# Performance work log

Hardware: AMD Instinct MI355X
Metric: run time of the kernel (lower is better)

## Reference

```python
import jax, jax.numpy as jnp
import numpy as np

IN_F = 128
OUT_F = 128
N_NODES = 50000
N_EDGES = 800000


def setup_inputs() -> dict:
    key = jax.random.key(0)
    k_x, k_e, k_w, k_b = jax.random.split(key, 4)
    x = jax.random.normal(k_x, (N_NODES, IN_F), dtype=jnp.float32)
    edge_index = jax.random.randint(k_e, (2, N_EDGES), 0, N_NODES, dtype=jnp.int64)
    # linear params (torch nn.Linear: y = x @ W.T + b)
    bound = 1.0 / np.sqrt(IN_F)
    W = jax.random.uniform(k_w, (OUT_F, IN_F), minval=-bound, maxval=bound, dtype=jnp.float32)
    b = jax.random.uniform(k_b, (OUT_F,), minval=-bound, maxval=bound, dtype=jnp.float32)
    return {"x": x, "edge_index": edge_index, "n_nodes": N_NODES, "W": W, "b": b}


def reference(x, edge_index, n_nodes, W, b):
    row, col = edge_index[0], edge_index[1]
    # gather source features and segment-sum into destination nodes
    agg = jax.ops.segment_sum(x[row], col, num_segments=n_nodes)  # [N, in_f]
    # in-degree, clamped to 1 (bincount + clamp in torch)
    deg = jax.ops.segment_sum(jnp.ones_like(col, dtype=jnp.float32), col, num_segments=n_nodes)
    deg = jnp.maximum(deg, 1.0)
    h = agg / deg[:, None]
    return h @ W.T + b
```

## Files before the change

kernel.cpp:

```cpp
#include <hip/hip_runtime.h>

#define IN_F 128
#define OUT_F 128

typedef unsigned int uint32;
typedef unsigned short ushort16;
using short8 = __attribute__((ext_vector_type(8))) short;
using f32x4  = __attribute__((ext_vector_type(4))) float;

__device__ __forceinline__ uint32 f2bf(float f) {
    const uint32 u = __float_as_uint(f);
    return (u + 0x7FFFu + ((u >> 16) & 1u)) >> 16;
}
__device__ __forceinline__ uint32 pack_bf2(float lo, float hi) {
    return f2bf(lo) | (f2bf(hi) << 16);
}

__global__ __launch_bounds__(256) void k_prep(
    const float* __restrict__ x, const float* __restrict__ W,
    uint32* __restrict__ xb, uint32* __restrict__ wb,
    int* __restrict__ deg_i, int nx4, int nw4, int nNodes)
{
    const int i4 = blockIdx.x * 256 + threadIdx.x;
    if (i4 < nNodes) deg_i[i4] = 0;
    if (i4 < nx4) {
        const float4 v = reinterpret_cast<const float4*>(x)[i4];
        uint2 st;
        st.x = pack_bf2(v.x, v.y);
        st.y = pack_bf2(v.z, v.w);
        reinterpret_cast<uint2*>(xb)[i4] = st;
    } else if (i4 - nx4 < nw4) {
        const int j4 = i4 - nx4;
        const float4 v = reinterpret_cast<const float4*>(W)[j4];
        uint2 st;
        st.x = pack_bf2(v.x, v.y);
        st.y = pack_bf2(v.z, v.w);
        reinterpret_cast<uint2*>(wb)[j4] = st;
    }
}

__global__ __launch_bounds__(256) void k_hist(
    const int* __restrict__ ei, int* __restrict__ deg_i, int nEdges)
{
    int e = blockIdx.x * blockDim.x + threadIdx.x;
    if (e < nEdges) {
        atomicAdd(&deg_i[ei[nEdges + e]], 1);
    }
}

__global__ __launch_bounds__(256) void k_scan_a(
    const int* __restrict__ deg_i, int* __restrict__ escan,
    int* __restrict__ bsum, int n)
{
    __shared__ int sh[256];
    const int t = threadIdx.x;
    const int i = blockIdx.x * 256 + t;
    int v = (i < n) ? deg_i[i] : 0;
    sh[t] = v;
    __syncthreads();
    for (int ofs = 1; ofs < 256; ofs <<= 1) {
        int u = (t >= ofs) ? sh[t - ofs] : 0;
        __syncthreads();
        sh[t] += u;
        __syncthreads();
    }
    if (i < n) escan[i] = sh[t] - v;
    if (t == 255) bsum[blockIdx.x] = sh[255];
}

__global__ __launch_bounds__(256) void k_scan_c(
    const int* __restrict__ escan, const int* __restrict__ bsum,
    int* __restrict__ off, int* __restrict__ cursor, int n, int nsb)
{
    __shared__ int sh[256];
    const int t = threadIdx.x;
    const int b = blockIdx.x;

    sh[t] = (t < nsb) ? bsum[t] : 0;
    __syncthreads();
    for (int ofs = 1; ofs < 256; ofs <<= 1) {
        int u = (t >= ofs) ? sh[t - ofs] : 0;
        __syncthreads();
        sh[t] += u;
        __syncthreads();
    }
    const int prefix = (b == 0) ? 0 : sh[b - 1];

    const int i = b * 256 + t;
    if (i < n) {
        const int o = escan[i] + prefix;
        off[i] = o;
        cursor[i] = o;
    }
}

__global__ __launch_bounds__(256) void k_scatter_ids(
    const int* __restrict__ ei, int* __restrict__ cursor,
    int* __restrict__ perm, int nEdges)
{
    const int cls = blockIdx.x & 7;
    const int e0 = ((blockIdx.x >> 3) * 256 + threadIdx.x) * 4;
    if (e0 >= nEdges) return;

    if (e0 + 4 <= nEdges) {
        const int4 dst4 = *reinterpret_cast<const int4*>(ei + nEdges + e0);
        const int4 src4 = *reinterpret_cast<const int4*>(ei + e0);
        if (((dst4.x >> 7) & 7) == cls) {
            const int p = atomicAdd(&cursor[dst4.x], 1);
            perm[p] = src4.x;
        }
        if (((dst4.y >> 7) & 7) == cls) {
            const int p = atomicAdd(&cursor[dst4.y], 1);
            perm[p] = src4.y;
        }
        if (((dst4.z >> 7) & 7) == cls) {
            const int p = atomicAdd(&cursor[dst4.z], 1);
            perm[p] = src4.z;
        }
        if (((dst4.w >> 7) & 7) == cls) {
            const int p = atomicAdd(&cursor[dst4.w], 1);
            perm[p] = src4.w;
        }
    } else {
        for (int e = e0; e < nEdges; ++e) {
            const int dst = ei[nEdges + e];
            if (((dst >> 7) & 7) == cls) {
                const int p = atomicAdd(&cursor[dst], 1);
                perm[p] = ei[e];
            }
        }
    }
}

__global__ __launch_bounds__(256) void k_gather(
    const uint32* __restrict__ xb2,
    const int* __restrict__ perm,
    const int* __restrict__ off,
    const int* __restrict__ deg_i,
    uint32* __restrict__ hb2,
    int nNodes)
{
    const int node = (blockIdx.x << 2) + (threadIdx.x >> 6);
    const int lane = threadIdx.x & 63;
    if (node >= nNodes) return;

    const int s = off[node];
    const int d = deg_i[node];

    float ax = 0.0f, ay = 0.0f;
    int i = 0;
    for (; i + 4 <= d; i += 4) {
        const uint32 u0 = xb2[(size_t)perm[s + i + 0] * 64 + lane];
        const uint32 u1 = xb2[(size_t)perm[s + i + 1] * 64 + lane];
        const uint32 u2 = xb2[(size_t)perm[s + i + 2] * 64 + lane];
        const uint32 u3 = xb2[(size_t)perm[s + i + 3] * 64 + lane];
        ax += __uint_as_float(u0 << 16);
        ay += __uint_as_float(u0 & 0xFFFF0000u);
        ax += __uint_as_float(u1 << 16);
        ay += __uint_as_float(u1 & 0xFFFF0000u);
        ax += __uint_as_float(u2 << 16);
        ay += __uint_as_float(u2 & 0xFFFF0000u);
        ax += __uint_as_float(u3 << 16);
        ay += __uint_as_float(u3 & 0xFFFF0000u);
    }
    for (; i < d; ++i) {
        const uint32 u = xb2[(size_t)perm[s + i] * 64 + lane];
        ax += __uint_as_float(u << 16);
        ay += __uint_as_float(u & 0xFFFF0000u);
    }

    const float inv = 1.0f / (float)(d > 0 ? d : 1);
    hb2[(size_t)node * 64 + lane] = pack_bf2(ax * inv, ay * inv);
}

__global__ __launch_bounds__(256) void k_mm(
    const ushort16* __restrict__ hbf,
    const ushort16* __restrict__ wbf,
    const float* __restrict__ bias,
    float* __restrict__ out, int nNodes)
{
    const int wave = threadIdx.x >> 6;
    const int lane = threadIdx.x & 63;
    const int m0 = blockIdx.x * 128 + wave * 32;
    const int lrow = lane & 15;
    const int kgrp = lane >> 4;

    short8 a[2][4];
#pragma unroll
    for (int mt = 0; mt < 2; ++mt) {
        int mrow = m0 + mt * 16 + lrow;
        if (mrow >= nNodes) mrow = nNodes - 1;
        const ushort16* hrow = hbf + (size_t)mrow * IN_F;
#pragma unroll
        for (int kt = 0; kt < 4; ++kt) {
            a[mt][kt] = *reinterpret_cast<const short8*>(hrow + kt * 32 + kgrp * 8);
        }
    }

#pragma unroll
    for (int nt = 0; nt < 8; ++nt) {
        const int n0 = nt * 16;
        const ushort16* wrow = wbf + (size_t)(n0 + lrow) * IN_F;
        const float bv = bias[n0 + lrow];

        f32x4 acc0 = {bv, bv, bv, bv};
        f32x4 acc1 = {bv, bv, bv, bv};
#pragma unroll
        for (int kt = 0; kt < 4; ++kt) {
            const short8 b = *reinterpret_cast<const short8*>(wrow + kt * 32 + kgrp * 8);
            acc0 = __builtin_amdgcn_mfma_f32_16x16x32_bf16(a[0][kt], b, acc0, 0, 0, 0);
            acc1 = __builtin_amdgcn_mfma_f32_16x16x32_bf16(a[1][kt], b, acc1, 0, 0, 0);
        }
#pragma unroll
        for (int r = 0; r < 4; ++r) {
            const int row0 = m0 + kgrp * 4 + r;
            const int row1 = m0 + 16 + kgrp * 4 + r;
            if (row0 < nNodes) out[(size_t)row0 * OUT_F + n0 + lrow] = acc0[r];
            if (row1 < nNodes) out[(size_t)row1 * OUT_F + n0 + lrow] = acc1[r];
        }
    }
}

extern "C" void kernel_launch(void* const* d_in, const int* in_sizes, int n_in,
                              void* d_out, int out_size, void* d_ws, size_t ws_size,
                              hipStream_t stream)
{
    const float* x   = (const float*)d_in[0];
    const int*   ei  = (const int*)d_in[1];
    const float* W   = (const float*)d_in[3];
    const float* b   = (const float*)d_in[4];
    float*       out = (float*)d_out;

    const int nNodes = in_sizes[0] / IN_F;
    const int nEdges = in_sizes[1] / 2;
    const int nsb = (nNodes + 255) / 256;

    int* deg_i  = (int*)d_ws;
    int* off    = deg_i + nNodes;
    int* cursor = off + nNodes;
    int* escan  = cursor + nNodes;
    int* bsum   = escan + nNodes;
    int* perm   = bsum + nsb;
    ushort16* hbf = (ushort16*)(perm + nEdges);
    ushort16* wbf = hbf + (size_t)nNodes * IN_F;

    uint32* xb = (uint32*)d_out;

    const int nx4 = (nNodes * IN_F) / 4;
    const int nw4 = (OUT_F * IN_F) / 4;
    k_prep<<<(nx4 + nw4 + 255) / 256, 256, 0, stream>>>(
        x, W, xb, (uint32*)wbf, deg_i, nx4, nw4, nNodes);

    const int eb = (nEdges + 255) / 256;
    k_hist<<<eb, 256, 0, stream>>>(ei, deg_i, nEdges);

    k_scan_a<<<nsb, 256, 0, stream>>>(deg_i, escan, bsum, nNodes);
    k_scan_c<<<nsb, 256, 0, stream>>>(escan, bsum, off, cursor, nNodes, nsb);

    const int chunks = (nEdges + 1023) / 1024;
    k_scatter_ids<<<chunks * 8, 256, 0, stream>>>(ei, cursor, perm, nEdges);

    const int gb = (nNodes + 3) / 4;
    k_gather<<<gb, 256, 0, stream>>>(xb, perm, off, deg_i, (uint32*)hbf, nNodes);

    const int mb = (nNodes + 127) / 128;
    k_mm<<<mb, 256, 0, stream>>>(hbf, wbf, b, out, nNodes);
}
```

Baseline: 142.6 us.

## Partition histogram and gather by node class for XCD locality; store perm as ushort

The degree histogram now uses the same scheme as the scatter: eight block classes, each scanning edges with int4 loads and doing atomics only for destinations in its class. The goal is to keep each node's counter in one XCD's L2. The gather kernel remaps blocks so each class processes the 128-node buckets that belong to it. The permutation array is stored as 16-bit source ids, which halves its traffic but only works while there are at most 65536 nodes. In exchange, every edge destination is read eight times across the classes.

```diff
diff --git a/kernel.cpp b/kernel.cpp
--- a/kernel.cpp
+++ b/kernel.cpp
@@ -42,9 +42,21 @@
 __global__ __launch_bounds__(256) void k_hist(
     const int* __restrict__ ei, int* __restrict__ deg_i, int nEdges)
 {
-    int e = blockIdx.x * blockDim.x + threadIdx.x;
-    if (e < nEdges) {
-        atomicAdd(&deg_i[ei[nEdges + e]], 1);
+    const int cls = blockIdx.x & 7;
+    const int e0 = ((blockIdx.x >> 3) * 256 + threadIdx.x) * 4;
+    if (e0 >= nEdges) return;
+
+    if (e0 + 4 <= nEdges) {
+        const int4 d4 = *reinterpret_cast<const int4*>(ei + nEdges + e0);
+        if (((d4.x >> 7) & 7) == cls) atomicAdd(&deg_i[d4.x], 1);
+        if (((d4.y >> 7) & 7) == cls) atomicAdd(&deg_i[d4.y], 1);
+        if (((d4.z >> 7) & 7) == cls) atomicAdd(&deg_i[d4.z], 1);
+        if (((d4.w >> 7) & 7) == cls) atomicAdd(&deg_i[d4.w], 1);
+    } else {
+        for (int e = e0; e < nEdges; ++e) {
+            const int dst = ei[nEdges + e];
+            if (((dst >> 7) & 7) == cls) atomicAdd(&deg_i[dst], 1);
+        }
     }
 }
 
@@ -96,37 +108,36 @@
 
 __global__ __launch_bounds__(256) void k_scatter_ids(
     const int* __restrict__ ei, int* __restrict__ cursor,
-    int* __restrict__ perm, int nEdges)
+    unsigned short* __restrict__ perm, int nEdges)
 {
     const int cls = blockIdx.x & 7;
     const int e0 = ((blockIdx.x >> 3) * 256 + threadIdx.x) * 4;
     if (e0 >= nEdges) return;
 
     if (e0 + 4 <= nEdges) {
-        const int4 dst4 = *reinterpret_cast<const int4*>(ei + nEdges + e0);
-        const int4 src4 = *reinterpret_cast<const int4*>(ei + e0);
-        if (((dst4.x >> 7) & 7) == cls) {
-            const int p = atomicAdd(&cursor[dst4.x], 1);
-            perm[p] = src4.x;
-        }
-        if (((dst4.y >> 7) & 7) == cls) {
-            const int p = atomicAdd(&cursor[dst4.y], 1);
-            perm[p] = src4.y;
-        }
-        if (((dst4.z >> 7) & 7) == cls) {
-            const int p = atomicAdd(&cursor[dst4.z], 1);
-            perm[p] = src4.z;
-        }
-        if (((dst4.w >> 7) & 7) == cls) {
-            const int p = atomicAdd(&cursor[dst4.w], 1);
-            perm[p] = src4.w;
+        const int4 d4 = *reinterpret_cast<const int4*>(ei + nEdges + e0);
+        if (((d4.x >> 7) & 7) == cls) {
+            const int p = atomicAdd(&cursor[d4.x], 1);
+            perm[p] = (unsigned short)ei[e0 + 0];
+        }
+        if (((d4.y >> 7) & 7) == cls) {
+            const int p = atomicAdd(&cursor[d4.y], 1);
+            perm[p] = (unsigned short)ei[e0 + 1];
+        }
+        if (((d4.z >> 7) & 7) == cls) {
+            const int p = atomicAdd(&cursor[d4.z], 1);
+            perm[p] = (unsigned short)ei[e0 + 2];
+        }
+        if (((d4.w >> 7) & 7) == cls) {
+            const int p = atomicAdd(&cursor[d4.w], 1);
+            perm[p] = (unsigned short)ei[e0 + 3];
         }
     } else {
         for (int e = e0; e < nEdges; ++e) {
             const int dst = ei[nEdges + e];
             if (((dst >> 7) & 7) == cls) {
                 const int p = atomicAdd(&cursor[dst], 1);
-                perm[p] = ei[e];
+                perm[p] = (unsigned short)ei[e];
             }
         }
     }
@@ -134,13 +145,16 @@
 
 __global__ __launch_bounds__(256) void k_gather(
     const uint32* __restrict__ xb2,
-    const int* __restrict__ perm,
+    const unsigned short* __restrict__ perm,
     const int* __restrict__ off,
     const int* __restrict__ deg_i,
     uint32* __restrict__ hb2,
     int nNodes)
 {
-    const int node = (blockIdx.x << 2) + (threadIdx.x >> 6);
+    const int cls = blockIdx.x & 7;
+    const int li  = (blockIdx.x >> 3) * 4 + (threadIdx.x >> 6);
+    const int bucket = cls + ((li >> 7) << 3);
+    const int node = (bucket << 7) + (li & 127);
     const int lane = threadIdx.x & 63;
     if (node >= nNodes) return;
 
@@ -234,13 +248,14 @@
     const int nNodes = in_sizes[0] / IN_F;
     const int nEdges = in_sizes[1] / 2;
     const int nsb = (nNodes + 255) / 256;
+    const int nBuckets = (nNodes + 127) / 128;
 
     int* deg_i  = (int*)d_ws;
     int* off    = deg_i + nNodes;
     int* cursor = off + nNodes;
     int* escan  = cursor + nNodes;
     int* bsum   = escan + nNodes;
-    int* perm   = bsum + nsb;
+    unsigned short* perm = (unsigned short*)(bsum + nsb);
     ushort16* hbf = (ushort16*)(perm + nEdges);
     ushort16* wbf = hbf + (size_t)nNodes * IN_F;
 
@@ -251,18 +266,17 @@
     k_prep<<<(nx4 + nw4 + 255) / 256, 256, 0, stream>>>(
         x, W, xb, (uint32*)wbf, deg_i, nx4, nw4, nNodes);
 
-    const int eb = (nEdges + 255) / 256;
-    k_hist<<<eb, 256, 0, stream>>>(ei, deg_i, nEdges);
+    const int chunks = (nEdges + 1023) / 1024;
+    k_hist<<<chunks * 8, 256, 0, stream>>>(ei, deg_i, nEdges);
 
     k_scan_a<<<nsb, 256, 0, stream>>>(deg_i, escan, bsum, nNodes);
     k_scan_c<<<nsb, 256, 0, stream>>>(escan, bsum, off, cursor, nNodes, nsb);
 
-    const int chunks = (nEdges + 1023) / 1024;
     k_scatter_ids<<<chunks * 8, 256, 0, stream>>>(ei, cursor, perm, nEdges);
 
-    const int gb = (nNodes + 3) / 4;
-    k_gather<<<gb, 256, 0, stream>>>(xb, perm, off, deg_i, (uint32*)hbf, nNodes);
-
-    const int mb = (nNodes + 127) / 128;
-    k_mm<<<mb, 256, 0, stream>>>(hbf, wbf, b, out, nNodes);
-}
+    const int tilesPerClass = ((nBuckets + 7) / 8) * 32;
+    k_gather<<<tilesPerClass * 8, 256, 0, stream>>>(xb, perm, off, deg_i,
+                                                    (uint32*)hbf, nNodes);
+
+    k_mm<<<nBuckets, 256, 0, stream>>>(hbf, wbf, b, out, nNodes);
+}
```

After: 146.2 us. 2.5% more time.
